# Kernel optimization log

Hardware: AMD Instinct MI355X
Metric: run time of the kernel (lower is better)

## Reference

```python
import jax, jax.numpy as jnp
import numpy as np

N, E, D, H = 50000, 800000, 128, 4
C = D // H  # per-head out channels
NEG_SLOPE = 0.2
BN_EPS = 1e-5


def _glorot(key, shape, fan):
    return jax.random.normal(key, shape, jnp.float32) / np.sqrt(fan)


def setup_inputs() -> dict:
    key = jax.random.key(0)
    ks = jax.random.split(key, 8)
    inp = {
        'x': jax.random.normal(ks[0], (N, D), jnp.float32),
        'edge_index': jax.random.randint(ks[1], (2, E), 0, N, dtype=jnp.int32),
        'Wl1': _glorot(ks[2], (D, D), D), 'Wr1': _glorot(ks[3], (D, D), D),
        'att1': _glorot(ks[4], (H, C), C), 'b1': jnp.zeros((D,), jnp.float32),
        'gamma1': jnp.ones((D,), jnp.float32), 'beta1': jnp.zeros((D,), jnp.float32),
        'Wl2': _glorot(ks[5], (D, D), D), 'Wr2': _glorot(ks[6], (D, D), D),
        'att2': _glorot(ks[7], (H, C), C), 'b2': jnp.zeros((D,), jnp.float32),
        'gamma2': jnp.ones((D,), jnp.float32), 'beta2': jnp.zeros((D,), jnp.float32),
    }
    return inp


def gatv2_conv(x, src, dst, Wl, Wr, att, bias):
    # PyG GATv2Conv, concat=True, add_self_loops handled by caller.
    n = x.shape[0]
    xl = (x @ Wl).reshape(n, H, C)  # source-side transform
    xr = (x @ Wr).reshape(n, H, C)  # target-side transform
    e = xl[src] + xr[dst]                      # [E', H, C]
    e = jnp.where(e > 0, e, NEG_SLOPE * e)     # LeakyReLU
    logits = jnp.einsum('ehc,hc->eh', e, att)  # [E', H]
    # segment softmax over destination node
    m = jax.ops.segment_max(logits, dst, num_segments=n)  # [N, H]
    ex = jnp.exp(logits - m[dst])
    den = jax.ops.segment_sum(ex, dst, num_segments=n)
    alpha = ex / den[dst]                      # [E', H]
    out = jax.ops.segment_sum(alpha[:, :, None] * xl[src], dst, num_segments=n)
    return out.reshape(n, H * C) + bias


def batchnorm(x, gamma, beta):
    mu = x.mean(0)
    var = x.var(0)
    return gamma * (x - mu) * jax.lax.rsqrt(var + BN_EPS) + beta


def reference(x, edge_index, Wl1, Wr1, att1, b1, gamma1, beta1,
              Wl2, Wr2, att2, b2, gamma2, beta2):
    n = x.shape[0]
    loop = jnp.arange(n, dtype=edge_index.dtype)
    src = jnp.concatenate([edge_index[0], loop])  # add self-loops (PyG default)
    dst = jnp.concatenate([edge_index[1], loop])
    identity = x
    out = gatv2_conv(x, src, dst, Wl1, Wr1, att1, b1)
    out = jax.nn.relu(batchnorm(out, gamma1, beta1))
    out = gatv2_conv(out, src, dst, Wl2, Wr2, att2, b2)
    out = batchnorm(out, gamma2, beta2) + identity
    return jax.nn.relu(out)
```

## Files before the change

kernel.cpp:

```cpp
#include <hip/hip_runtime.h>
#include <cstdint>
#include <cstddef>

#define D 128
#define BN_EPS 1e-5f
#define NEG_INF -3.0e38f
#define BN_BLOCKS 512

typedef __attribute__((ext_vector_type(8))) short bf16x8;
typedef __attribute__((ext_vector_type(4))) float f32x4;

static __device__ __forceinline__ unsigned short f2bf(float f) {
    uint32_t u = __float_as_uint(f);
    uint32_t r = (u + 0x7fffu + ((u >> 16) & 1u)) >> 16;
    return (unsigned short)r;
}

static __device__ __forceinline__ float qsum4(float x) {
    x += __int_as_float(__builtin_amdgcn_update_dpp(0, __float_as_int(x), 0xB1, 0xF, 0xF, true));
    x += __int_as_float(__builtin_amdgcn_update_dpp(0, __float_as_int(x), 0x4E, 0xF, 0xF, true));
    return x;
}

__global__ void zero_kernel(int* cnt, int n, unsigned short* esrc_tail) {
    int i = blockIdx.x * 256 + threadIdx.x;
    if (i < n) cnt[i] = 0;
    if (i < 16) esrc_tail[i] = 0;
}

__global__ void hist_kernel(const int* __restrict__ dst, int* __restrict__ cnt, int E) {
    int e = blockIdx.x * 256 + threadIdx.x;
    if (e < E) atomicAdd(&cnt[dst[e]], 1);
}

__global__ void scan_block(const int* __restrict__ cnt, int* __restrict__ row_start,
                           int* __restrict__ bsum, int n) {
    __shared__ int tmp[256];
    int tid = threadIdx.x;
    int i = blockIdx.x * 256 + tid;
    int v = (i < n) ? cnt[i] : 0;
    tmp[tid] = v; __syncthreads();
    for (int off = 1; off < 256; off <<= 1) {
        int t = (tid >= off) ? tmp[tid - off] : 0;
        __syncthreads();
        tmp[tid] += t; __syncthreads();
    }
    if (i < n) row_start[i + 1] = tmp[tid];
    if (tid == 255) bsum[blockIdx.x] = tmp[255];
}

__global__ void scan_bsum(int* bsum, int nb) {
    __shared__ int tmp[256];
    int tid = threadIdx.x;
    int v = (tid < nb) ? bsum[tid] : 0;
    tmp[tid] = v; __syncthreads();
    for (int off = 1; off < 256; off <<= 1) {
        int t = (tid >= off) ? tmp[tid - off] : 0;
        __syncthreads();
        tmp[tid] += t; __syncthreads();
    }
    if (tid < nb) bsum[tid] = tmp[tid];
}

__global__ void scan_fix(int* __restrict__ row_start, const int* __restrict__ bsum,
                         int* __restrict__ cursor, int n) {
    int i = blockIdx.x * 256 + threadIdx.x;
    if (i < n) {
        int add = (blockIdx.x > 0) ? bsum[blockIdx.x - 1] : 0;
        int val = row_start[i + 1] + add;
        row_start[i + 1] = val;
        if (i + 1 < n) cursor[i + 1] = val;
    }
    if (i == 0) { row_start[0] = 0; cursor[0] = 0; }
}

__global__ void scatter_kernel(const int* __restrict__ src, const int* __restrict__ dst,
                               int* __restrict__ cursor, unsigned short* __restrict__ esrc, int E) {
    int e = blockIdx.x * 256 + threadIdx.x;
    if (e < E) {
        int p = atomicAdd(&cursor[dst[e]], 1);
        esrc[p] = (unsigned short)src[e];
    }
}

__global__ void repack_w(const float* __restrict__ Wl, const float* __restrict__ Wr,
                         unsigned short* __restrict__ Bp) {
    int idx = blockIdx.x * 256 + threadIdx.x;
    int i    = idx & 7;
    int lane = (idx >> 3) & 63;
    int kt   = (idx >> 9) & 3;
    int jt   = idx >> 11;
    int k   = kt * 32 + (lane >> 4) * 8 + i;
    int col = jt * 16 + (lane & 15);
    float v = (col < 128) ? Wl[k * 128 + col] : Wr[k * 128 + (col - 128)];
    Bp[idx] = f2bf(v);
}

template<bool BN>
__global__ __launch_bounds__(256, 2) void gemm_mfma(
    const float* __restrict__ X, const unsigned short* __restrict__ Bp,
    const float* __restrict__ scale, const float* __restrict__ shift,
    unsigned short* __restrict__ xl, float* __restrict__ xr, int n)
{
    __shared__ unsigned short smem[32768];
    {
        const float4* s = (const float4*)Bp;
        float4* d = (float4*)smem;
        #pragma unroll
        for (int it = 0; it < 16; ++it)
            d[it * 256 + threadIdx.x] = s[it * 256 + threadIdx.x];
    }
    __syncthreads();

    int wid = threadIdx.x >> 6, lane = threadIdx.x & 63;
    int nw = (n + 31) >> 5;
    int wrow = blockIdx.x * 4 + wid;
    if (wrow >= nw) return;
    int r0 = wrow * 32;
    int m = lane & 15, hi = lane >> 4;

    f32x4 accA[16], accB[16];
    #pragma unroll
    for (int jt = 0; jt < 16; ++jt) {
        accA[jt] = (f32x4){0.f, 0.f, 0.f, 0.f};
        accB[jt] = (f32x4){0.f, 0.f, 0.f, 0.f};
    }

    int rA = r0 + m;      if (rA > n - 1) rA = n - 1;
    int rB = r0 + 16 + m; if (rB > n - 1) rB = n - 1;
    const float* xrowA = X + (size_t)rA * D;
    const float* xrowB = X + (size_t)rB * D;

    #pragma unroll
    for (int kt = 0; kt < 4; ++kt) {
        int kb = kt * 32 + hi * 8;
        float sca[8], shf[8];
        if (BN) {
            float4 s0 = *(const float4*)(scale + kb);
            float4 s1 = *(const float4*)(scale + kb + 4);
            float4 h0 = *(const float4*)(shift + kb);
            float4 h1 = *(const float4*)(shift + kb + 4);
            sca[0]=s0.x; sca[1]=s0.y; sca[2]=s0.z; sca[3]=s0.w;
            sca[4]=s1.x; sca[5]=s1.y; sca[6]=s1.z; sca[7]=s1.w;
            shf[0]=h0.x; shf[1]=h0.y; shf[2]=h0.z; shf[3]=h0.w;
            shf[4]=h1.x; shf[5]=h1.y; shf[6]=h1.z; shf[7]=h1.w;
        }
        float4 a0 = *(const float4*)(xrowA + kb);
        float4 a1 = *(const float4*)(xrowA + kb + 4);
        float4 b0 = *(const float4*)(xrowB + kb);
        float4 b1 = *(const float4*)(xrowB + kb + 4);
        float avA[8] = {a0.x, a0.y, a0.z, a0.w, a1.x, a1.y, a1.z, a1.w};
        float avB[8] = {b0.x, b0.y, b0.z, b0.w, b1.x, b1.y, b1.z, b1.w};
        bf16x8 afragA, afragB;
        #pragma unroll
        for (int i = 0; i < 8; ++i) {
            float va = avA[i], vb = avB[i];
            if (BN) {
                va = fmaxf(va * sca[i] + shf[i], 0.f);
                vb = fmaxf(vb * sca[i] + shf[i], 0.f);
            }
            afragA[i] = (short)f2bf(va);
            afragB[i] = (short)f2bf(vb);
        }
        #pragma unroll
        for (int jt = 0; jt < 16; ++jt) {
            bf16x8 bfrag = *(const bf16x8*)(smem + (size_t)((jt * 4 + kt) * 64 + lane) * 8);
            accA[jt] = __builtin_amdgcn_mfma_f32_16x16x32_bf16(afragA, bfrag, accA[jt], 0, 0, 0);
            accB[jt] = __builtin_amdgcn_mfma_f32_16x16x32_bf16(afragB, bfrag, accB[jt], 0, 0, 0);
        }
    }

    #pragma unroll
    for (int jt = 0; jt < 16; ++jt) {
        int col = jt * 16 + m;
        #pragma unroll
        for (int r = 0; r < 4; ++r) {
            int rowA = r0 + hi * 4 + r;
            int rowB = rowA + 16;
            if (rowA < n) {
                float v = accA[jt][r];
                if (jt < 8) xl[(size_t)rowA * D + col] = f2bf(v);
                else        xr[(size_t)rowA * D + (col - 128)] = v;
            }
            if (rowB < n) {
                float v = accB[jt][r];
                if (jt < 8) xl[(size_t)rowB * D + col] = f2bf(v);
                else        xr[(size_t)rowB * D + (col - 128)] = v;
            }
        }
    }
}

__global__ __launch_bounds__(256) void gat_kernel(
    const unsigned short* __restrict__ xl, const float* __restrict__ xr,
    const float* __restrict__ att, const float* __restrict__ bias,
    const int* __restrict__ row_start, const unsigned short* __restrict__ esrc,
    float* __restrict__ h, int n)
{
    const float L2E = 1.44269504089f;
    int wid = threadIdx.x >> 6;
    int lane = threadIdx.x & 63;
    int v = blockIdx.x * 4 + wid;
    if (v >= n) return;
    int g  = lane >> 4;
    int il = lane & 15;

    float xrv[8], av[8];
    {
        float4 xa = *(const float4*)(xr + (size_t)v * D + il * 8);
        float4 xb = *(const float4*)(xr + (size_t)v * D + il * 8 + 4);
        xrv[0]=xa.x; xrv[1]=xa.y; xrv[2]=xa.z; xrv[3]=xa.w;
        xrv[4]=xb.x; xrv[5]=xb.y; xrv[6]=xb.z; xrv[7]=xb.w;
        float4 aa = *(const float4*)(att + il * 8);
        float4 ab = *(const float4*)(att + il * 8 + 4);
        av[0]=aa.x*L2E; av[1]=aa.y*L2E; av[2]=aa.z*L2E; av[3]=aa.w*L2E;
        av[4]=ab.x*L2E; av[5]=ab.y*L2E; av[6]=ab.z*L2E; av[7]=ab.w*L2E;
    }

    int p = row_start[v];
    int deg = row_start[v + 1] - p;
    int vcnt = deg + 1;

    float m = NEG_INF, den = 0.f;
    float acc[8] = {0.f, 0.f, 0.f, 0.f, 0.f, 0.f, 0.f, 0.f};

    auto unpack = [](uint4 q, float* x) {
        x[0] = __uint_as_float(q.x << 16); x[1] = __uint_as_float(q.x & 0xffff0000u);
        x[2] = __uint_as_float(q.y << 16); x[3] = __uint_as_float(q.y & 0xffff0000u);
        x[4] = __uint_as_float(q.z << 16); x[5] = __uint_as_float(q.z & 0xffff0000u);
        x[6] = __uint_as_float(q.w << 16); x[7] = __uint_as_float(q.w & 0xffff0000u);
    };
    auto logit = [&](const float* x) {
        float d = 0.f;
        #pragma unroll
        for (int k = 0; k < 8; ++k) {
            float f = x[k] + xrv[k];
            f = fmaxf(f, 0.2f * f);
            d = fmaf(av[k], f, d);
        }
        return qsum4(d);
    };

    {
        uint32_t u0 = (g == 0) ? (uint32_t)v : (uint32_t)esrc[p + g - 1];
        bool val0 = g < vcnt;
        uint4 q0 = *(const uint4*)(xl + ((size_t)u0 << 7) + il * 8);
        float x[8]; unpack(q0, x);
        float lg = val0 ? logit(x) : NEG_INF;
        if (__any(lg > m + 8.f)) { m = fmaxf(m, lg); }
        float pex = val0 ? exp2f(lg - m) : 0.f;
        den += pex;
        #pragma unroll
        for (int k = 0; k < 8; ++k) acc[k] = fmaf(pex, x[k], acc[k]);
    }
    for (int base = 4; base < vcnt; base += 8) {
        int iA = base + g, iB = base + 4 + g;
        bool vA = iA < vcnt, vB = iB < vcnt;
        uint32_t uA = vA ? (uint32_t)esrc[p + iA - 1] : 0u;
        uint32_t uB = vB ? (uint32_t)esrc[p + iB - 1] : 0u;
        uint4 qA = *(const uint4*)(xl + ((size_t)uA << 7) + il * 8);
        uint4 qB = *(const uint4*)(xl + ((size_t)uB << 7) + il * 8);
        float xA[8], xB[8];
        unpack(qA, xA); unpack(qB, xB);
        float lgA = logit(xA); lgA = vA ? lgA : NEG_INF;
        float lgB = logit(xB); lgB = vB ? lgB : NEG_INF;
        float mx = fmaxf(lgA, lgB);
        if (__any(mx > m + 8.f)) {
            float nm = fmaxf(m, mx);
            float sc = exp2f(m - nm);
            den *= sc;
            #pragma unroll
            for (int k = 0; k < 8; ++k) acc[k] *= sc;
            m = nm;
        }
        float pA = exp2f(lgA - m);
        float pB = exp2f(lgB - m);
        den += pA + pB;
        #pragma unroll
        for (int k = 0; k < 8; ++k)
            acc[k] = fmaf(pA, xA[k], fmaf(pB, xB[k], acc[k]));
    }

    float m2 = fmaxf(m, __shfl_xor(m, 16));
    float M  = fmaxf(m2, __shfl_xor(m2, 32));
    float sc = exp2f(m - M);
    den *= sc;
    den += __shfl_xor(den, 16);
    den += __shfl_xor(den, 32);
    #pragma unroll
    for (int k = 0; k < 8; ++k) {
        acc[k] *= sc;
        acc[k] += __shfl_xor(acc[k], 16);
        acc[k] += __shfl_xor(acc[k], 32);
    }
    if (g == 0) {
        float inv = 1.f / den;
        float4 ba = *(const float4*)(bias + il * 8);
        float4 bb = *(const float4*)(bias + il * 8 + 4);
        float4 o0, o1;
        o0.x = fmaf(acc[0], inv, ba.x); o0.y = fmaf(acc[1], inv, ba.y);
        o0.z = fmaf(acc[2], inv, ba.z); o0.w = fmaf(acc[3], inv, ba.w);
        o1.x = fmaf(acc[4], inv, bb.x); o1.y = fmaf(acc[5], inv, bb.y);
        o1.z = fmaf(acc[6], inv, bb.z); o1.w = fmaf(acc[7], inv, bb.w);
        *(float4*)(h + (size_t)v * D + il * 8)     = o0;
        *(float4*)(h + (size_t)v * D + il * 8 + 4) = o1;
    }
}

__global__ __launch_bounds__(256) void bn_stats(const float* __restrict__ h,
                                                float* __restrict__ psum, float* __restrict__ psum2, int n)
{
    int c4 = threadIdx.x & 31;
    int ty = threadIdx.x >> 5;
    float sx = 0.f, sy = 0.f, sz = 0.f, sw = 0.f;
    float qx = 0.f, qy = 0.f, qz = 0.f, qw = 0.f;
    for (int r = blockIdx.x * 8 + ty; r < n; r += gridDim.x * 8) {
        float4 v = *(const float4*)(h + (size_t)r * D + c4 * 4);
        sx += v.x; sy += v.y; sz += v.z; sw += v.w;
        qx = fmaf(v.x, v.x, qx); qy = fmaf(v.y, v.y, qy);
        qz = fmaf(v.z, v.z, qz); qw = fmaf(v.w, v.w, qw);
    }
    __shared__ float4 smA[256], smB[256];
    smA[threadIdx.x] = make_float4(sx, sy, sz, sw);
    smB[threadIdx.x] = make_float4(qx, qy, qz, qw);
    __syncthreads();
    #pragma unroll
    for (int off = 128; off >= 32; off >>= 1) {
        if (threadIdx.x < off) {
            float4 a = smA[threadIdx.x], b = smA[threadIdx.x + off];
            smA[threadIdx.x] = make_float4(a.x + b.x, a.y + b.y, a.z + b.z, a.w + b.w);
            float4 c = smB[threadIdx.x], d2 = smB[threadIdx.x + off];
            smB[threadIdx.x] = make_float4(c.x + d2.x, c.y + d2.y, c.z + d2.z, c.w + d2.w);
        }
        __syncthreads();
    }
    if (threadIdx.x < 32) {
        ((float4*)psum)[blockIdx.x * 32 + threadIdx.x]  = smA[threadIdx.x];
        ((float4*)psum2)[blockIdx.x * 32 + threadIdx.x] = smB[threadIdx.x];
    }
}

__global__ __launch_bounds__(256) void bn_mid(const float* __restrict__ psum, const float* __restrict__ psum2,
                                              float* __restrict__ pmid, float* __restrict__ pmid2)
{
    int c4 = threadIdx.x & 31;
    int rg = threadIdx.x >> 5;
    float4 s = make_float4(0.f, 0.f, 0.f, 0.f), q = make_float4(0.f, 0.f, 0.f, 0.f);
    #pragma unroll
    for (int k = 0; k < 4; ++k) {
        int r = blockIdx.x * 32 + rg + k * 8;
        float4 a = ((const float4*)psum)[r * 32 + c4];
        float4 b = ((const float4*)psum2)[r * 32 + c4];
        s.x += a.x; s.y += a.y; s.z += a.z; s.w += a.w;
        q.x += b.x; q.y += b.y; q.z += b.z; q.w += b.w;
    }
    __shared__ float4 smA[256], smB[256];
    smA[threadIdx.x] = s; smB[threadIdx.x] = q;
    __syncthreads();
    #pragma unroll
    for (int off = 128; off >= 32; off >>= 1) {
        if (threadIdx.x < off) {
            float4 a = smA[threadIdx.x], b = smA[threadIdx.x + off];
            smA[threadIdx.x] = make_float4(a.x + b.x, a.y + b.y, a.z + b.z, a.w + b.w);
            float4 c = smB[threadIdx.x], d2 = smB[threadIdx.x + off];
            smB[threadIdx.x] = make_float4(c.x + d2.x, c.y + d2.y, c.z + d2.z, c.w + d2.w);
        }
        __syncthreads();
    }
    if (threadIdx.x < 32) {
        ((float4*)pmid)[blockIdx.x * 32 + threadIdx.x]  = smA[threadIdx.x];
        ((float4*)pmid2)[blockIdx.x * 32 + threadIdx.x] = smB[threadIdx.x];
    }
}

__global__ void bn_final(const float* __restrict__ psum, const float* __restrict__ psum2,
                         const float* __restrict__ gamma, const float* __restrict__ beta,
                         float* __restrict__ scale, float* __restrict__ shift,
                         float inv_n, int nblk)
{
    int c = threadIdx.x & 127;
    int half = threadIdx.x >> 7;
    float s = 0.f, s2 = 0.f;
    for (int b = half; b < nblk; b += 2) {
        s  += psum[b * 128 + c];
        s2 += psum2[b * 128 + c];
    }
    __shared__ float sm[256], sm2[256];
    sm[threadIdx.x] = s; sm2[threadIdx.x] = s2; __syncthreads();
    if (half == 0) {
        s  += sm[threadIdx.x + 128];
        s2 += sm2[threadIdx.x + 128];
        float mu = s * inv_n;
        float var = s2 * inv_n - mu * mu;
        float inv = rsqrtf(var + BN_EPS);
        float sc = gamma[c] * inv;
        scale[c] = sc;
        shift[c] = beta[c] - mu * sc;
    }
}

__global__ __launch_bounds__(256) void final_kernel(
    const float* __restrict__ h2, const float* __restrict__ x,
    const float* __restrict__ scale, const float* __restrict__ shift,
    float* __restrict__ out, int total)
{
    int i = blockIdx.x * 256 + threadIdx.x;
    if (i * 4 >= total) return;
    float4 hv = ((const float4*)h2)[i];
    float4 xv = ((const float4*)x)[i];
    int c = (i * 4) & 127;
    float4 o;
    o.x = fmaxf(hv.x * scale[c + 0] + shift[c + 0] + xv.x, 0.f);
    o.y = fmaxf(hv.y * scale[c + 1] + shift[c + 1] + xv.y, 0.f);
    o.z = fmaxf(hv.z * scale[c + 2] + shift[c + 2] + xv.z, 0.f);
    o.w = fmaxf(hv.w * scale[c + 3] + shift[c + 3] + xv.w, 0.f);
    ((float4*)out)[i] = o;
}

extern "C" void kernel_launch(void* const* d_in, const int* in_sizes, int n_in,
                              void* d_out, int out_size, void* d_ws, size_t ws_size,
                              hipStream_t stream)
{
    const float* x    = (const float*)d_in[0];
    const int*   ei   = (const int*)  d_in[1];
    const float* Wl1  = (const float*)d_in[2];
    const float* Wr1  = (const float*)d_in[3];
    const float* att1 = (const float*)d_in[4];
    const float* b1   = (const float*)d_in[5];
    const float* g1   = (const float*)d_in[6];
    const float* be1  = (const float*)d_in[7];
    const float* Wl2  = (const float*)d_in[8];
    const float* Wr2  = (const float*)d_in[9];
    const float* att2 = (const float*)d_in[10];
    const float* b2   = (const float*)d_in[11];
    const float* g2   = (const float*)d_in[12];
    const float* be2  = (const float*)d_in[13];
    float* out = (float*)d_out;

    int n = in_sizes[0] / D;
    int E = in_sizes[1] / 2;
    const int* e_src = ei;
    const int* e_dst = ei + E;

    char* w = (char*)d_ws;
    auto alloc = [&](size_t bytes) -> char* {
        char* p = w;
        w += (bytes + 255) / 256 * 256;
        return p;
    };
    unsigned short* xl = (unsigned short*)alloc((size_t)n * D * 2);
    float* xr          = (float*)alloc((size_t)n * D * 4);
    float* h           = (float*)alloc((size_t)n * D * 4);
    int* row_start     = (int*)alloc((size_t)(n + 1) * 4);
    int* cnt           = (int*)alloc((size_t)n * 4);
    int* cursor        = (int*)alloc((size_t)n * 4);
    unsigned short* esrc = (unsigned short*)alloc((size_t)(E + 16) * 2);
    int* bsum          = (int*)alloc(256 * 4);
    float* bn          = (float*)alloc(4 * 128 * 4);
    float* psum        = (float*)alloc((size_t)BN_BLOCKS * 128 * 4);
    float* psum2       = (float*)alloc((size_t)BN_BLOCKS * 128 * 4);
    float* pmid        = (float*)alloc(16 * 128 * 4);
    float* pmid2       = (float*)alloc(16 * 128 * 4);
    unsigned short* Bp1 = (unsigned short*)alloc(32768 * 2);
    unsigned short* Bp2 = (unsigned short*)alloc(32768 * 2);

    int nb = (n + 255) / 256;
    int gemm_blocks = (((n + 31) / 32) + 3) / 4;

    zero_kernel<<<(n + 255) / 256, 256, 0, stream>>>(cnt, n, esrc + E);
    hist_kernel<<<(E + 255) / 256, 256, 0, stream>>>(e_dst, cnt, E);
    scan_block<<<nb, 256, 0, stream>>>(cnt, row_start, bsum, n);
    scan_bsum<<<1, 256, 0, stream>>>(bsum, nb);
    scan_fix<<<nb, 256, 0, stream>>>(row_start, bsum, cursor, n);
    scatter_kernel<<<(E + 255) / 256, 256, 0, stream>>>(e_src, e_dst, cursor, esrc, E);
    repack_w<<<128, 256, 0, stream>>>(Wl1, Wr1, Bp1);
    repack_w<<<128, 256, 0, stream>>>(Wl2, Wr2, Bp2);

    gemm_mfma<false><<<gemm_blocks, 256, 0, stream>>>(x, Bp1, nullptr, nullptr, xl, xr, n);
    gat_kernel<<<(n + 3) / 4, 256, 0, stream>>>(xl, xr, att1, b1, row_start, esrc, h, n);
    bn_stats<<<BN_BLOCKS, 256, 0, stream>>>(h, psum, psum2, n);
    bn_mid<<<16, 256, 0, stream>>>(psum, psum2, pmid, pmid2);
    bn_final<<<1, 256, 0, stream>>>(pmid, pmid2, g1, be1, bn + 0, bn + 128, 1.0f / n, 16);

    gemm_mfma<true><<<gemm_blocks, 256, 0, stream>>>(h, Bp2, bn + 0, bn + 128, xl, xr, n);
    gat_kernel<<<(n + 3) / 4, 256, 0, stream>>>(xl, xr, att2, b2, row_start, esrc, h, n);
    bn_stats<<<BN_BLOCKS, 256, 0, stream>>>(h, psum, psum2, n);
    bn_mid<<<16, 256, 0, stream>>>(psum, psum2, pmid, pmid2);
    bn_final<<<1, 256, 0, stream>>>(pmid, pmid2, g2, be2, bn + 256, bn + 384, 1.0f / n, 16);

    final_kernel<<<((n * D / 4) + 255) / 256, 256, 0, stream>>>(h, x, bn + 256, bn + 384, out, n * D);
}
```

Baseline: 265.6 us.

## Sort nodes by degree, fold self-loops into CSR, rewrite LeakyReLU as abs

Self-loops now become ordinary CSR entries: counts start at one and scan_fix writes each node's own index first. This removes the special first iteration in the GAT loop. Three new kernels (degree histogram, scan, scatter) build a permutation that groups nodes by degree, so waves in a block get similar work and divergence and tail imbalance drop. LeakyReLU is rewritten as 0.6*f + 0.4*|f| folded into the attention weights, replacing fmax with fabs plus two FMAs. The cost is extra preprocessing launches, an extra indirection through perm, and node order that is no longer sequential, which can hurt locality of the xr and h accesses.

```diff
diff --git a/kernel.cpp b/kernel.cpp
--- a/kernel.cpp
+++ b/kernel.cpp
@@ -5,6 +5,7 @@
 #define D 128
 #define BN_EPS 1e-5f
 #define NEG_INF -3.0e38f
+#define M_INIT  -1.0e30f
 #define BN_BLOCKS 512
 
 typedef __attribute__((ext_vector_type(8))) short bf16x8;
@@ -22,9 +23,10 @@
     return x;
 }
 
-__global__ void zero_kernel(int* cnt, int n, unsigned short* esrc_tail) {
+__global__ void zero_kernel(int* cnt, int n, int* ghist, unsigned short* esrc_tail) {
     int i = blockIdx.x * 256 + threadIdx.x;
-    if (i < n) cnt[i] = 0;
+    if (i < n) cnt[i] = 1;
+    if (i < 256) ghist[i] = 0;
     if (i < 16) esrc_tail[i] = 0;
 }
 
@@ -63,15 +65,18 @@
 }
 
 __global__ void scan_fix(int* __restrict__ row_start, const int* __restrict__ bsum,
-                         int* __restrict__ cursor, int n) {
+                         int* __restrict__ cursor, unsigned short* __restrict__ esrc, int n) {
     int i = blockIdx.x * 256 + threadIdx.x;
     if (i < n) {
         int add = (blockIdx.x > 0) ? bsum[blockIdx.x - 1] : 0;
         int val = row_start[i + 1] + add;
         row_start[i + 1] = val;
-        if (i + 1 < n) cursor[i + 1] = val;
-    }
-    if (i == 0) { row_start[0] = 0; cursor[0] = 0; }
+        if (i + 1 < n) {
+            cursor[i + 1] = val + 1;
+            esrc[val] = (unsigned short)(i + 1);
+        }
+    }
+    if (i == 0) { row_start[0] = 0; cursor[0] = 1; esrc[0] = 0; }
 }
 
 __global__ void scatter_kernel(const int* __restrict__ src, const int* __restrict__ dst,
@@ -81,6 +86,50 @@
         int p = atomicAdd(&cursor[dst[e]], 1);
         esrc[p] = (unsigned short)src[e];
     }
+}
+
+__global__ void dhist_kernel(const int* __restrict__ row_start, int* __restrict__ ghist, int n) {
+    __shared__ int lh[256];
+    int tid = threadIdx.x;
+    lh[tid] = 0; __syncthreads();
+    for (int i = blockIdx.x * 256 + tid; i < n; i += gridDim.x * 256) {
+        int vc = row_start[i + 1] - row_start[i];
+        atomicAdd(&lh[vc < 255 ? vc : 255], 1);
+    }
+    __syncthreads();
+    if (lh[tid] > 0) atomicAdd(&ghist[tid], lh[tid]);
+}
+
+__global__ void dscan_kernel(const int* __restrict__ ghist, int* __restrict__ dcursor) {
+    __shared__ int tmp[256];
+    int tid = threadIdx.x;
+    int v = ghist[tid];
+    tmp[tid] = v; __syncthreads();
+    for (int off = 1; off < 256; off <<= 1) {
+        int t = (tid >= off) ? tmp[tid - off] : 0;
+        __syncthreads();
+        tmp[tid] += t; __syncthreads();
+    }
+    dcursor[tid] = tmp[tid] - v;
+}
+
+__global__ void dscatter_kernel(const int* __restrict__ row_start, int* __restrict__ dcursor,
+                                unsigned short* __restrict__ perm, int n) {
+    __shared__ int lh[256], lbase[256];
+    int tid = threadIdx.x;
+    int i = blockIdx.x * 256 + tid;
+    lh[tid] = 0; __syncthreads();
+    int b = 0, r = 0;
+    bool ok = i < n;
+    if (ok) {
+        int vc = row_start[i + 1] - row_start[i];
+        b = vc < 255 ? vc : 255;
+        r = atomicAdd(&lh[b], 1);
+    }
+    __syncthreads();
+    if (lh[tid] > 0) lbase[tid] = atomicAdd(&dcursor[tid], lh[tid]);
+    __syncthreads();
+    if (ok) perm[lbase[b] + r] = (unsigned short)i;
 }
 
 __global__ void repack_w(const float* __restrict__ Wl, const float* __restrict__ Wr,
@@ -195,17 +244,19 @@
     const unsigned short* __restrict__ xl, const float* __restrict__ xr,
     const float* __restrict__ att, const float* __restrict__ bias,
     const int* __restrict__ row_start, const unsigned short* __restrict__ esrc,
+    const unsigned short* __restrict__ perm,
     float* __restrict__ h, int n)
 {
     const float L2E = 1.44269504089f;
     int wid = threadIdx.x >> 6;
     int lane = threadIdx.x & 63;
-    int v = blockIdx.x * 4 + wid;
-    if (v >= n) return;
+    int idx = blockIdx.x * 4 + wid;
+    if (idx >= n) return;
+    int v = perm[idx];
     int g  = lane >> 4;
     int il = lane & 15;
 
-    float xrv[8], av[8];
+    float xrv[8], a06[8], a04[8];
     {
         float4 xa = *(const float4*)(xr + (size_t)v * D + il * 8);
         float4 xb = *(const float4*)(xr + (size_t)v * D + il * 8 + 4);
@@ -213,15 +264,18 @@
         xrv[4]=xb.x; xrv[5]=xb.y; xrv[6]=xb.z; xrv[7]=xb.w;
         float4 aa = *(const float4*)(att + il * 8);
         float4 ab = *(const float4*)(att + il * 8 + 4);
-        av[0]=aa.x*L2E; av[1]=aa.y*L2E; av[2]=aa.z*L2E; av[3]=aa.w*L2E;
-        av[4]=ab.x*L2E; av[5]=ab.y*L2E; av[6]=ab.z*L2E; av[7]=ab.w*L2E;
+        float t[8] = {aa.x, aa.y, aa.z, aa.w, ab.x, ab.y, ab.z, ab.w};
+        #pragma unroll
+        for (int k = 0; k < 8; ++k) {
+            a06[k] = 0.6f * L2E * t[k];
+            a04[k] = 0.4f * L2E * t[k];
+        }
     }
 
     int p = row_start[v];
-    int deg = row_start[v + 1] - p;
-    int vcnt = deg + 1;
-
-    float m = NEG_INF, den = 0.f;
+    int vcnt = row_start[v + 1] - p;
+
+    float m = M_INIT, den = 0.f;
     float acc[8] = {0.f, 0.f, 0.f, 0.f, 0.f, 0.f, 0.f, 0.f};
 
     auto unpack = [](uint4 q, float* x) {
@@ -231,33 +285,21 @@
         x[6] = __uint_as_float(q.w << 16); x[7] = __uint_as_float(q.w & 0xffff0000u);
     };
     auto logit = [&](const float* x) {
-        float d = 0.f;
+        float d0 = 0.f, d1 = 0.f;
         #pragma unroll
         for (int k = 0; k < 8; ++k) {
             float f = x[k] + xrv[k];
-            f = fmaxf(f, 0.2f * f);
-            d = fmaf(av[k], f, d);
-        }
-        return qsum4(d);
+            d0 = fmaf(a06[k], f, d0);
+            d1 = fmaf(a04[k], fabsf(f), d1);
+        }
+        return qsum4(d0 + d1);
     };
 
-    {
-        uint32_t u0 = (g == 0) ? (uint32_t)v : (uint32_t)esrc[p + g - 1];
-        bool val0 = g < vcnt;
-        uint4 q0 = *(const uint4*)(xl + ((size_t)u0 << 7) + il * 8);
-        float x[8]; unpack(q0, x);
-        float lg = val0 ? logit(x) : NEG_INF;
-        if (__any(lg > m + 8.f)) { m = fmaxf(m, lg); }
-        float pex = val0 ? exp2f(lg - m) : 0.f;
-        den += pex;
-        #pragma unroll
-        for (int k = 0; k < 8; ++k) acc[k] = fmaf(pex, x[k], acc[k]);
-    }
-    for (int base = 4; base < vcnt; base += 8) {
-        int iA = base + g, iB = base + 4 + g;
+    for (int base = 0; base < vcnt; base += 8) {
+        int iA = base + g, iB = iA + 4;
         bool vA = iA < vcnt, vB = iB < vcnt;
-        uint32_t uA = vA ? (uint32_t)esrc[p + iA - 1] : 0u;
-        uint32_t uB = vB ? (uint32_t)esrc[p + iB - 1] : 0u;
+        uint32_t uA = (uint32_t)esrc[p + iA];
+        uint32_t uB = (uint32_t)esrc[p + iB];
         uint4 qA = *(const uint4*)(xl + ((size_t)uA << 7) + il * 8);
         uint4 qB = *(const uint4*)(xl + ((size_t)uB << 7) + il * 8);
         float xA[8], xB[8];
@@ -454,8 +496,11 @@
     int* row_start     = (int*)alloc((size_t)(n + 1) * 4);
     int* cnt           = (int*)alloc((size_t)n * 4);
     int* cursor        = (int*)alloc((size_t)n * 4);
-    unsigned short* esrc = (unsigned short*)alloc((size_t)(E + 16) * 2);
+    unsigned short* esrc = (unsigned short*)alloc((size_t)(E + n + 16) * 2);
     int* bsum          = (int*)alloc(256 * 4);
+    int* ghist         = (int*)alloc(256 * 4);
+    int* dcursor       = (int*)alloc(256 * 4);
+    unsigned short* perm = (unsigned short*)alloc((size_t)n * 2);
     float* bn          = (float*)alloc(4 * 128 * 4);
     float* psum        = (float*)alloc((size_t)BN_BLOCKS * 128 * 4);
     float* psum2       = (float*)alloc((size_t)BN_BLOCKS * 128 * 4);
@@ -467,23 +512,26 @@
     int nb = (n + 255) / 256;
     int gemm_blocks = (((n + 31) / 32) + 3) / 4;
 
-    zero_kernel<<<(n + 255) / 256, 256, 0, stream>>>(cnt, n, esrc + E);
+    zero_kernel<<<nb, 256, 0, stream>>>(cnt, n, ghist, esrc + E + n);
     hist_kernel<<<(E + 255) / 256, 256, 0, stream>>>(e_dst, cnt, E);
     scan_block<<<nb, 256, 0, stream>>>(cnt, row_start, bsum, n);
     scan_bsum<<<1, 256, 0, stream>>>(bsum, nb);
-    scan_fix<<<nb, 256, 0, stream>>>(row_start, bsum, cursor, n);
+    scan_fix<<<nb, 256, 0, stream>>>(row_start, bsum, cursor, esrc, n);
     scatter_kernel<<<(E + 255) / 256, 256, 0, stream>>>(e_src, e_dst, cursor, esrc, E);
+    dhist_kernel<<<64, 256, 0, stream>>>(row_start, ghist, n);
+    dscan_kernel<<<1, 256, 0, stream>>>(ghist, dcursor);
+    dscatter_kernel<<<nb, 256, 0, stream>>>(row_start, dcursor, perm, n);
     repack_w<<<128, 256, 0, stream>>>(Wl1, Wr1, Bp1);
     repack_w<<<128, 256, 0, stream>>>(Wl2, Wr2, Bp2);
 
     gemm_mfma<false><<<gemm_blocks, 256, 0, stream>>>(x, Bp1, nullptr, nullptr, xl, xr, n);
-    gat_kernel<<<(n + 3) / 4, 256, 0, stream>>>(xl, xr, att1, b1, row_start, esrc, h, n);
+    gat_kernel<<<(n + 3) / 4, 256, 0, stream>>>(xl, xr, att1, b1, row_start, esrc, perm, h, n);
     bn_stats<<<BN_BLOCKS, 256, 0, stream>>>(h, psum, psum2, n);
     bn_mid<<<16, 256, 0, stream>>>(psum, psum2, pmid, pmid2);
     bn_final<<<1, 256, 0, stream>>>(pmid, pmid2, g1, be1, bn + 0, bn + 128, 1.0f / n, 16);
 
     gemm_mfma<true><<<gemm_blocks, 256, 0, stream>>>(h, Bp2, bn + 0, bn + 128, xl, xr, n);
-    gat_kernel<<<(n + 3) / 4, 256, 0, stream>>>(xl, xr, att2, b2, row_start, esrc, h, n);
+    gat_kernel<<<(n + 3) / 4, 256, 0, stream>>>(xl, xr, att2, b2, row_start, esrc, perm, h, n);
     bn_stats<<<BN_BLOCKS, 256, 0, stream>>>(h, psum, psum2, n);
     bn_mid<<<16, 256, 0, stream>>>(psum, psum2, pmid, pmid2);
     bn_final<<<1, 256, 0, stream>>>(pmid, pmid2, g2, be2, bn + 256, bn + 384, 1.0f / n, 16);
```

Measured after the change: 270.7 us. No clear change (+2.0%).
